# Kernel optimization log

Measured on AMD Instinct MI355X. Metric: run time of the kernel, lower is better.

The kernel has to match this reference:

```python
import jax, jax.numpy as jnp
import numpy as np

B, N, K, F = 1, 50000, 16, 128
EPS = 1e-5

def _bn(h, gamma, beta):
    # BatchNorm1d in training mode: per-feature-channel stats over (batch, nodes)
    mean = jnp.mean(h, axis=(0, 1), keepdims=True)
    var = jnp.var(h, axis=(0, 1), keepdims=True)
    return (h - mean) * jax.lax.rsqrt(var + EPS) * gamma + beta

def _rgcn(h, neighbors, W, b):
    # pad one zero node row, gather K neighbors per node, flatten, linear
    h_pad = jnp.pad(h, ((0, 0), (0, 1), (0, 0)))           # [B, N+1, F]
    gathered = h_pad[:, neighbors]                          # [B, N, K, F]
    flat = gathered.reshape(h.shape[0], neighbors.shape[0], -1)  # [B, N, K*F]
    return jnp.einsum('bnk,ok->bno', flat, W) + b

def setup_inputs():
    key = jax.random.key(0)
    ks = jax.random.split(key, 10)
    x = jax.random.normal(ks[0], (B, N, F), jnp.float32)
    graph = jax.random.randint(ks[1], (N, K, 2), 0, N)
    gamma1 = 1.0 + 0.1 * jax.random.normal(ks[2], (F,), jnp.float32)
    beta1 = 0.1 * jax.random.normal(ks[3], (F,), jnp.float32)
    gamma2 = 1.0 + 0.1 * jax.random.normal(ks[4], (F,), jnp.float32)
    beta2 = 0.1 * jax.random.normal(ks[5], (F,), jnp.float32)
    s = 1.0 / np.sqrt(K * F)
    W1 = jax.random.uniform(ks[6], (F, K * F), jnp.float32, -s, s)
    b1 = jax.random.uniform(ks[7], (F,), jnp.float32, -s, s)
    W2 = jax.random.uniform(ks[8], (F, K * F), jnp.float32, -s, s)
    b2 = jax.random.uniform(ks[9], (F,), jnp.float32, -s, s)
    return {"x": x, "graph": graph, "gamma1": gamma1, "beta1": beta1,
            "W1": W1, "b1": b1, "gamma2": gamma2, "beta2": beta2,
            "W2": W2, "b2": b2}

def reference(x, graph, gamma1, beta1, W1, b1, gamma2, beta2, W2, b2):
    neighbors = graph[..., 1]                               # [N, K]
    out = jax.nn.gelu(_bn(x, gamma1, beta1), approximate=False)
    out = _rgcn(out, neighbors, W1, b1)                     # [B, N, F]
    out = jax.nn.gelu(_bn(out, gamma2, beta2), approximate=False)
    out = _rgcn(out, neighbors, W2, b2)                     # [B, N, F]
    return out + x
```

## Files before the change

kernel.cpp:

```cpp
#include <hip/hip_runtime.h>


#define NN  50000
#define NB  500
#define NPB 100

typedef __bf16 v8bf __attribute__((ext_vector_type(8)));
typedef unsigned short u8s __attribute__((ext_vector_type(8)));
typedef float  v4f  __attribute__((ext_vector_type(4)));
typedef float  vf2  __attribute__((ext_vector_type(2)));

__device__ __forceinline__ unsigned short f2bf(float f) {
  unsigned int u = __builtin_bit_cast(unsigned int, f);
  u += 0x7FFFu + ((u >> 16) & 1u);
  return (unsigned short)(u >> 16);
}
__device__ __forceinline__ float bf2f(unsigned short s) {
  unsigned int u = ((unsigned int)s) << 16;
  return __builtin_bit_cast(float, u);
}
__device__ __forceinline__ float gelu_f(float y) {
  return 0.5f * y * (1.0f + erff(y * 0.70710678118654752f));
}

__device__ __forceinline__ v8bf fp8x8_to_bf16x8(unsigned int lo, unsigned int hi) {
  vf2 f0 = __builtin_amdgcn_cvt_pk_f32_fp8((int)lo, false);
  vf2 f1 = __builtin_amdgcn_cvt_pk_f32_fp8((int)lo, true);
  vf2 f2 = __builtin_amdgcn_cvt_pk_f32_fp8((int)hi, false);
  vf2 f3 = __builtin_amdgcn_cvt_pk_f32_fp8((int)hi, true);
  unsigned int d0, d1, d2, d3;
  asm("v_cvt_pk_bf16_f32 %0, %1, %2" : "=v"(d0) : "v"(f0.x), "v"(f0.y));
  asm("v_cvt_pk_bf16_f32 %0, %1, %2" : "=v"(d1) : "v"(f1.x), "v"(f1.y));
  asm("v_cvt_pk_bf16_f32 %0, %1, %2" : "=v"(d2) : "v"(f2.x), "v"(f2.y));
  asm("v_cvt_pk_bf16_f32 %0, %1, %2" : "=v"(d3) : "v"(f3.x), "v"(f3.y));
  uint4 u = make_uint4(d0, d1, d2, d3);
  return __builtin_bit_cast(v8bf, u);
}

__global__ void wconv_kernel(const float* __restrict__ W1, const float* __restrict__ W2,
                             unsigned short* __restrict__ Wt1, unsigned short* __restrict__ Wt2) {
  int t = blockIdx.x * 256 + threadIdx.x;
  const bool is2 = (t >= 32768);
  const float* W = is2 ? W2 : W1;
  unsigned short* Wt = is2 ? Wt2 : Wt1;
  int r = t & 32767;
  int frag = r >> 6, lane = r & 63;
  int k4 = frag >> 3, c = frag & 7;
  int o  = c * 16 + (lane & 15);
  int lq = lane >> 4;
  int kd;
  if (!is2) {
    kd = k4 * 32 + lq * 8;
  } else {
    int s_ = k4 >> 2, w_ = k4 & 3;
    kd = s_ * 128 + (w_ >> 1) * 64 + lq * 16 + (w_ & 1) * 8;
  }
  const float* src = W + o * 2048 + kd;
  unsigned short* dst = Wt + r * 8;
#pragma unroll
  for (int j = 0; j < 8; ++j) dst[j] = f2bf(src[j]);
}

__global__ void bn_stats_kernel(const float* __restrict__ x, float* __restrict__ part) {
  float s0=0,s1=0,s2=0,s3=0,q0=0,q1=0,q2=0,q3=0;
  for (int cb = blockIdx.x; cb < (NN*128/1024); cb += 256) {
    float4 v = reinterpret_cast<const float4*>(x)[cb * 256 + threadIdx.x];
    s0+=v.x; q0+=v.x*v.x; s1+=v.y; q1+=v.y*v.y;
    s2+=v.z; q2+=v.z*v.z; s3+=v.w; q3+=v.w*v.w;
  }
  __shared__ float ls[1024], lsq[1024];
  int fb = (threadIdx.x & 31) * 4;
  int sl = threadIdx.x >> 5;
  ls[sl*128+fb]   = s0; ls[sl*128+fb+1]  = s1; ls[sl*128+fb+2]  = s2; ls[sl*128+fb+3]  = s3;
  lsq[sl*128+fb]  = q0; lsq[sl*128+fb+1] = q1; lsq[sl*128+fb+2] = q2; lsq[sl*128+fb+3] = q3;
  __syncthreads();
  if (threadIdx.x < 128) {
    float S=0,Q=0;
#pragma unroll
    for (int s2i=0; s2i<8; ++s2i){ S += ls[s2i*128+threadIdx.x]; Q += lsq[s2i*128+threadIdx.x]; }
    part[blockIdx.x*256 + threadIdx.x]       = S;
    part[blockIdx.x*256 + 128 + threadIdx.x] = Q;
  }
}

__global__ __launch_bounds__(1024) void bn_reduce_kernel(
    const float* __restrict__ part, int nb,
    const float* __restrict__ gamma, const float* __restrict__ beta,
    float* __restrict__ scsh) {
  int f = threadIdx.x & 127;
  int g = threadIdx.x >> 7;
  float S = 0.f, Q = 0.f;
  for (int b = g; b < nb; b += 8) {
    S += part[b * 256 + f];
    Q += part[b * 256 + 128 + f];
  }
  __shared__ float ls[8][128], lq[8][128];
  ls[g][f] = S; lq[g][f] = Q;
  __syncthreads();
  if (threadIdx.x < 128) {
    float St = 0.f, Qt = 0.f;
#pragma unroll
    for (int i = 0; i < 8; ++i) { St += ls[i][f]; Qt += lq[i][f]; }
    float inv  = 1.0f / (float)NN;
    float mean = St * inv;
    float var  = fmaxf(Qt * inv - mean * mean, 0.0f);
    float sc   = gamma[f] * rsqrtf(var + 1e-5f);
    scsh[f]       = sc;
    scsh[128 + f] = beta[f] - mean * sc;
  }
}

__global__ void apply1_kernel(const float* __restrict__ x, const float* __restrict__ scsh,
                              unsigned short* __restrict__ h1) {
  int stride = gridDim.x * blockDim.x;
  for (int c = blockIdx.x * blockDim.x + threadIdx.x; c < NN*128/4; c += stride) {
    float4 v = reinterpret_cast<const float4*>(x)[c];
    int f = (c * 4) & 127;
    ushort4 o;
    o.x = f2bf(gelu_f(v.x * scsh[f]   + scsh[128+f]));
    o.y = f2bf(gelu_f(v.y * scsh[f+1] + scsh[128+f+1]));
    o.z = f2bf(gelu_f(v.z * scsh[f+2] + scsh[128+f+2]));
    o.w = f2bf(gelu_f(v.w * scsh[f+3] + scsh[128+f+3]));
    reinterpret_cast<ushort4*>(h1)[c] = o;
  }
}

__global__ void apply2_kernel(const unsigned short* __restrict__ t1,
                              const float* __restrict__ scsh,
                              unsigned int* __restrict__ h2) {
  int stride = gridDim.x * blockDim.x;
  for (int c = blockIdx.x * blockDim.x + threadIdx.x; c < NN*128/8; c += stride) {
    u8s v = reinterpret_cast<const u8s*>(t1)[c];
    int f = (c * 8) & 127;
    float r[8];
#pragma unroll
    for (int j = 0; j < 8; ++j)
      r[j] = gelu_f(bf2f((unsigned short)v[j]) * scsh[f + j] + scsh[128 + f + j]);
    int lo = __builtin_amdgcn_cvt_pk_fp8_f32(r[0], r[1], 0,  false);
    lo     = __builtin_amdgcn_cvt_pk_fp8_f32(r[2], r[3], lo, true);
    int hi = __builtin_amdgcn_cvt_pk_fp8_f32(r[4], r[5], 0,  false);
    hi     = __builtin_amdgcn_cvt_pk_fp8_f32(r[6], r[7], hi, true);
    reinterpret_cast<uint2*>(h2)[c] = make_uint2((unsigned)lo, (unsigned)hi);
  }
}

template<int MODE>
__global__ __launch_bounds__(256, 2) void rgcn_kernel(
    const void* __restrict__ hb,
    const unsigned short* __restrict__ Wt,
    const int* __restrict__ graph,
    const float* __restrict__ bias,
    const float* __restrict__ xres,
    float* __restrict__ outf,
    unsigned short* __restrict__ outb,
    float* __restrict__ part)
{
  __shared__ unsigned short bsm[16384];
  __shared__ float lds_s[4][128];
  __shared__ float lds_q[4][128];

  const unsigned short* h16 = (const unsigned short*)hb;
  const unsigned char*  h8  = (const unsigned char*)hb;

  const int tid  = threadIdx.x;
  const int wv   = tid >> 6;
  const int lane = tid & 63;
  const int l15  = lane & 15;
  const int lq   = lane >> 4;
  const int nb0  = blockIdx.x * NPB;

  v4f acc[2][8];
#pragma unroll
  for (int rf = 0; rf < 2; ++rf)
#pragma unroll
    for (int c = 0; c < 8; ++c) acc[rf][c] = (v4f){0.f, 0.f, 0.f, 0.f};

  const int an0 = min(nb0 + wv * 32 + l15,      NN - 1);
  const int an1 = min(nb0 + wv * 32 + 16 + l15, NN - 1);

  int idx0[16], idx1[16];
  {
    const int4* g0 = reinterpret_cast<const int4*>(graph + an0 * 32);
    const int4* g1 = reinterpret_cast<const int4*>(graph + an1 * 32);
#pragma unroll
    for (int j = 0; j < 8; ++j) {
      int4 t0 = g0[j], t1v = g1[j];
      idx0[2*j]   = min(max(t0.y,  0), NN - 1) * 128;
      idx0[2*j+1] = min(max(t0.w,  0), NN - 1) * 128;
      idx1[2*j]   = min(max(t1v.y, 0), NN - 1) * 128;
      idx1[2*j+1] = min(max(t1v.w, 0), NN - 1) * 128;
    }
  }

  v8bf  A0[2][4],  A1[2][4];
  uint4 A0u[2][2], A1u[2][2];

#define LOADA(buf_, s_) {                                                 \
    if constexpr (MODE == 0) {                                            \
      const unsigned short* r0 = h16 + idx0[s_] + lq * 8;                 \
      const unsigned short* r1 = h16 + idx1[s_] + lq * 8;                 \
      _Pragma("unroll")                                                   \
      for (int w4 = 0; w4 < 4; ++w4) {                                    \
        A0[buf_][w4] = *reinterpret_cast<const v8bf*>(r0 + w4 * 32);      \
        A1[buf_][w4] = *reinterpret_cast<const v8bf*>(r1 + w4 * 32);      \
      }                                                                   \
    } else {                                                              \
      const unsigned char* r0 = h8 + idx0[s_] + lq * 16;                  \
      const unsigned char* r1 = h8 + idx1[s_] + lq * 16;                  \
      A0u[buf_][0] = *reinterpret_cast<const uint4*>(r0);                 \
      A0u[buf_][1] = *reinterpret_cast<const uint4*>(r0 + 64);            \
      A1u[buf_][0] = *reinterpret_cast<const uint4*>(r1);                 \
      A1u[buf_][1] = *reinterpret_cast<const uint4*>(r1 + 64);            \
    }                                                                     \
  }

#define STAGE(s_) {                                                           \
    const unsigned short* gsrc = Wt + (s_) * 16384 + wv * 4096 + lane * 8;    \
    unsigned short* ldst = &bsm[wv * 4096];                                   \
    _Pragma("unroll")                                                         \
    for (int i = 0; i < 8; ++i) {                                             \
      __builtin_amdgcn_global_load_lds(                                       \
        (const __attribute__((address_space(1))) void*)(gsrc + i * 512),      \
        (__attribute__((address_space(3))) void*)(ldst + i * 512),            \
        16, 0, 0);                                                            \
    }                                                                         \
  }

#define SLOT(s_) {                                                            \
    if ((s_) < 15) LOADA(((s_) + 1) & 1, ((s_) + 1) & 15)                     \
    __builtin_amdgcn_sched_barrier(0);                                        \
    __builtin_amdgcn_s_setprio(1);                                            \
    {                                                                         \
      const int cur_ = (s_) & 1;                                              \
      _Pragma("unroll")                                                       \
      for (int w4 = 0; w4 < 4; ++w4) {                                        \
        v8bf a0v, a1v;                                                        \
        if constexpr (MODE == 0) {                                            \
          a0v = A0[cur_][w4];                                                 \
          a1v = A1[cur_][w4];                                                 \
        } else {                                                              \
          uint4 u0 = A0u[cur_][w4 >> 1];                                      \
          uint4 u1 = A1u[cur_][w4 >> 1];                                      \
          if ((w4 & 1) == 0) {                                                \
            a0v = fp8x8_to_bf16x8(u0.x, u0.y);                                \
            a1v = fp8x8_to_bf16x8(u1.x, u1.y);                                \
          } else {                                                            \
            a0v = fp8x8_to_bf16x8(u0.z, u0.w);                                \
            a1v = fp8x8_to_bf16x8(u1.z, u1.w);                                \
          }                                                                   \
        }                                                                     \
        _Pragma("unroll")                                                     \
        for (int c = 0; c < 8; ++c) {                                         \
          v8bf b = *reinterpret_cast<const v8bf*>(                            \
              &bsm[(w4 * 8 + c) * 512 + lane * 8]);                           \
          acc[0][c] = __builtin_amdgcn_mfma_f32_16x16x32_bf16(                \
                        a0v, b, acc[0][c], 0, 0, 0);                          \
          acc[1][c] = __builtin_amdgcn_mfma_f32_16x16x32_bf16(                \
                        a1v, b, acc[1][c], 0, 0, 0);                          \
        }                                                                     \
      }                                                                       \
    }                                                                         \
    __builtin_amdgcn_s_setprio(0);                                            \
    __builtin_amdgcn_sched_barrier(0);                                        \
    __builtin_amdgcn_s_barrier();             \
    __builtin_amdgcn_sched_barrier(0);                                        \
    if ((s_) < 15) STAGE(((s_) + 1) & 15)                                     \
    __syncthreads();                      \
  }

  STAGE(0)
  LOADA(0, 0)
  __syncthreads();

  SLOT(0)  SLOT(1)  SLOT(2)  SLOT(3)
  SLOT(4)  SLOT(5)  SLOT(6)  SLOT(7)
  SLOT(8)  SLOT(9)  SLOT(10) SLOT(11)
  SLOT(12) SLOT(13) SLOT(14) SLOT(15)
#undef SLOT
#undef LOADA
#undef STAGE

  if constexpr (MODE == 0) {
#pragma unroll
    for (int c = 0; c < 8; ++c) {
      float s = 0.f, q = 0.f;
#pragma unroll
      for (int rf = 0; rf < 2; ++rf) {
#pragma unroll
        for (int j = 0; j < 4; ++j) {
          int lrow = wv * 32 + rf * 16 + lq * 4 + j;
          float v  = acc[rf][c][j];
          if (lrow < NPB) { s += v; q += v * v; }
          bsm[lrow * 128 + c * 16 + l15] = f2bf(v);
        }
      }
      s += __shfl_xor(s, 16, 64); s += __shfl_xor(s, 32, 64);
      q += __shfl_xor(q, 16, 64); q += __shfl_xor(q, 32, 64);
      if (lq == 0) { lds_s[wv][c * 16 + l15] = s; lds_q[wv][c * 16 + l15] = q; }
    }
    __syncthreads();
    unsigned short* t1b = outb + nb0 * 128;
#pragma unroll
    for (int i = 0; i < 7; ++i) {
      int off = i * 2048 + tid * 8;
      if (off < NPB * 128) {
        *reinterpret_cast<u8s*>(t1b + off) =
            *reinterpret_cast<const u8s*>(&bsm[off]);
      }
    }
    if (tid < 128) {
      float S = lds_s[0][tid] + lds_s[1][tid] + lds_s[2][tid] + lds_s[3][tid];
      float Q = lds_q[0][tid] + lds_q[1][tid] + lds_q[2][tid] + lds_q[3][tid];
      part[blockIdx.x * 256 + tid]       = S;
      part[blockIdx.x * 256 + 128 + tid] = Q;
    }
  } else {
#pragma unroll
    for (int c = 0; c < 8; ++c) {
      float bv = bias[c * 16 + l15];
#pragma unroll
      for (int rf = 0; rf < 2; ++rf) {
#pragma unroll
        for (int j = 0; j < 4; ++j) {
          int node = nb0 + wv * 32 + rf * 16 + lq * 4 + j;
          if (node < nb0 + NPB) {
            int idx = node * 128 + c * 16 + l15;
            outf[idx] = acc[rf][c][j] + bv + xres[idx];
          }
        }
      }
    }
  }
}

extern "C" void kernel_launch(void* const* d_in, const int* in_sizes, int n_in,
                              void* d_out, int out_size, void* d_ws, size_t ws_size,
                              hipStream_t stream) {
  const float* x      = (const float*)d_in[0];
  const int*   graph  = (const int*)d_in[1];
  const float* gamma1 = (const float*)d_in[2];
  const float* beta1  = (const float*)d_in[3];
  const float* W1     = (const float*)d_in[4];
  const float* gamma2 = (const float*)d_in[6];
  const float* beta2  = (const float*)d_in[7];
  const float* W2     = (const float*)d_in[8];
  const float* b2     = (const float*)d_in[9];
  float* out = (float*)d_out;

  char* ws = (char*)d_ws;
  unsigned short* h1  = (unsigned short*)(ws);
  unsigned short* t1  = (unsigned short*)(ws + 12800000);
  unsigned short* Wt1 = (unsigned short*)(ws + 25600000);
  unsigned short* Wt2 = (unsigned short*)(ws + 26124288);
  float* p1    = (float*)(ws + 26648576);
  float* p2    = (float*)(ws + 26910720);
  float* scsh1 = (float*)(ws + 27422720);
  float* scsh2 = (float*)(ws + 27423744);

  wconv_kernel<<<256, 256, 0, stream>>>(W1, W2, Wt1, Wt2);
  bn_stats_kernel<<<256, 256, 0, stream>>>(x, p1);
  bn_reduce_kernel<<<1, 1024, 0, stream>>>(p1, 256, gamma1, beta1, scsh1);
  apply1_kernel<<<2048, 256, 0, stream>>>(x, scsh1, h1);
  rgcn_kernel<0><<<NB, 256, 0, stream>>>(h1, Wt1, graph, nullptr, nullptr,
                                         nullptr, t1, p2);
  bn_reduce_kernel<<<1, 1024, 0, stream>>>(p2, NB, gamma2, beta2, scsh2);
  apply2_kernel<<<2048, 256, 0, stream>>>(t1, scsh2, (unsigned int*)h1);
  rgcn_kernel<1><<<NB, 256, 0, stream>>>(h1, Wt2, graph, b2, x,
                                         out, nullptr, nullptr);
}
```

Before: 201.3 us.

## Store first-layer activations in FP8 and process two neighbor slots per pipeline phase

The first GELU output is now stored as FP8 instead of bf16, so both RGCN layers share the FP8 gather path and weight layout. This halves the bytes of the random neighbor gathers in layer one. The main loop now handles two neighbor slots per phase with a doubled LDS weight buffer, which halves the number of barriers and stage steps. The cost is lower precision in the first layer's inputs and 64KB of LDS per block, which may reduce occupancy below the two blocks per CU the launch bounds request.

Measured after the change: 203.6 us. No clear change (+1.2%).

```diff
diff --git a/kernel.cpp b/kernel.cpp
--- a/kernel.cpp
+++ b/kernel.cpp
@@ -48,13 +48,8 @@
   int k4 = frag >> 3, c = frag & 7;
   int o  = c * 16 + (lane & 15);
   int lq = lane >> 4;
-  int kd;
-  if (!is2) {
-    kd = k4 * 32 + lq * 8;
-  } else {
-    int s_ = k4 >> 2, w_ = k4 & 3;
-    kd = s_ * 128 + (w_ >> 1) * 64 + lq * 16 + (w_ & 1) * 8;
-  }
+  int s_ = k4 >> 2, w_ = k4 & 3;
+  int kd = s_ * 128 + (w_ >> 1) * 64 + lq * 16 + (w_ & 1) * 8;
   const float* src = W + o * 2048 + kd;
   unsigned short* dst = Wt + r * 8;
 #pragma unroll
@@ -111,17 +106,21 @@
 }
 
 __global__ void apply1_kernel(const float* __restrict__ x, const float* __restrict__ scsh,
-                              unsigned short* __restrict__ h1) {
+                              unsigned int* __restrict__ h1) {
   int stride = gridDim.x * blockDim.x;
-  for (int c = blockIdx.x * blockDim.x + threadIdx.x; c < NN*128/4; c += stride) {
-    float4 v = reinterpret_cast<const float4*>(x)[c];
-    int f = (c * 4) & 127;
-    ushort4 o;
-    o.x = f2bf(gelu_f(v.x * scsh[f]   + scsh[128+f]));
-    o.y = f2bf(gelu_f(v.y * scsh[f+1] + scsh[128+f+1]));
-    o.z = f2bf(gelu_f(v.z * scsh[f+2] + scsh[128+f+2]));
-    o.w = f2bf(gelu_f(v.w * scsh[f+3] + scsh[128+f+3]));
-    reinterpret_cast<ushort4*>(h1)[c] = o;
+  for (int c = blockIdx.x * blockDim.x + threadIdx.x; c < NN*128/8; c += stride) {
+    float4 v0 = reinterpret_cast<const float4*>(x)[c * 2];
+    float4 v1 = reinterpret_cast<const float4*>(x)[c * 2 + 1];
+    int f = (c * 8) & 127;
+    float r[8] = {v0.x, v0.y, v0.z, v0.w, v1.x, v1.y, v1.z, v1.w};
+#pragma unroll
+    for (int j = 0; j < 8; ++j)
+      r[j] = gelu_f(r[j] * scsh[f + j] + scsh[128 + f + j]);
+    int lo = __builtin_amdgcn_cvt_pk_fp8_f32(r[0], r[1], 0,  false);
+    lo     = __builtin_amdgcn_cvt_pk_fp8_f32(r[2], r[3], lo, true);
+    int hi = __builtin_amdgcn_cvt_pk_fp8_f32(r[4], r[5], 0,  false);
+    hi     = __builtin_amdgcn_cvt_pk_fp8_f32(r[6], r[7], hi, true);
+    reinterpret_cast<uint2*>(h1)[c] = make_uint2((unsigned)lo, (unsigned)hi);
   }
 }
 
@@ -146,7 +145,7 @@
 
 template<int MODE>
 __global__ __launch_bounds__(256, 2) void rgcn_kernel(
-    const void* __restrict__ hb,
+    const unsigned char* __restrict__ h8,
     const unsigned short* __restrict__ Wt,
     const int* __restrict__ graph,
     const float* __restrict__ bias,
@@ -155,12 +154,9 @@
     unsigned short* __restrict__ outb,
     float* __restrict__ part)
 {
-  __shared__ unsigned short bsm[16384];
+  __shared__ unsigned short bsm[32768];
   __shared__ float lds_s[4][128];
   __shared__ float lds_q[4][128];
-
-  const unsigned short* h16 = (const unsigned short*)hb;
-  const unsigned char*  h8  = (const unsigned char*)hb;
 
   const int tid  = threadIdx.x;
   const int wv   = tid >> 6;
@@ -192,33 +188,25 @@
     }
   }
 
-  v8bf  A0[2][4],  A1[2][4];
-  uint4 A0u[2][2], A1u[2][2];
-
-#define LOADA(buf_, s_) {                                                 \
-    if constexpr (MODE == 0) {                                            \
-      const unsigned short* r0 = h16 + idx0[s_] + lq * 8;                 \
-      const unsigned short* r1 = h16 + idx1[s_] + lq * 8;                 \
-      _Pragma("unroll")                                                   \
-      for (int w4 = 0; w4 < 4; ++w4) {                                    \
-        A0[buf_][w4] = *reinterpret_cast<const v8bf*>(r0 + w4 * 32);      \
-        A1[buf_][w4] = *reinterpret_cast<const v8bf*>(r1 + w4 * 32);      \
-      }                                                                   \
-    } else {                                                              \
-      const unsigned char* r0 = h8 + idx0[s_] + lq * 16;                  \
-      const unsigned char* r1 = h8 + idx1[s_] + lq * 16;                  \
-      A0u[buf_][0] = *reinterpret_cast<const uint4*>(r0);                 \
-      A0u[buf_][1] = *reinterpret_cast<const uint4*>(r0 + 64);            \
-      A1u[buf_][0] = *reinterpret_cast<const uint4*>(r1);                 \
-      A1u[buf_][1] = *reinterpret_cast<const uint4*>(r1 + 64);            \
+  uint4 A0u[2][2][2], A1u[2][2][2];
+
+#define LOADA2(buf_, p_) {                                                \
+    _Pragma("unroll")                                                     \
+    for (int sl = 0; sl < 2; ++sl) {                                      \
+      const unsigned char* r0 = h8 + idx0[(p_) * 2 + sl] + lq * 16;       \
+      const unsigned char* r1 = h8 + idx1[(p_) * 2 + sl] + lq * 16;       \
+      A0u[buf_][sl][0] = *reinterpret_cast<const uint4*>(r0);             \
+      A0u[buf_][sl][1] = *reinterpret_cast<const uint4*>(r0 + 64);        \
+      A1u[buf_][sl][0] = *reinterpret_cast<const uint4*>(r1);             \
+      A1u[buf_][sl][1] = *reinterpret_cast<const uint4*>(r1 + 64);        \
     }                                                                     \
   }
 
-#define STAGE(s_) {                                                           \
-    const unsigned short* gsrc = Wt + (s_) * 16384 + wv * 4096 + lane * 8;    \
-    unsigned short* ldst = &bsm[wv * 4096];                                   \
+#define STAGE2(p_) {                                                          \
+    const unsigned short* gsrc = Wt + (p_) * 32768 + wv * 8192 + lane * 8;    \
+    unsigned short* ldst = &bsm[wv * 8192];                                   \
     _Pragma("unroll")                                                         \
-    for (int i = 0; i < 8; ++i) {                                             \
+    for (int i = 0; i < 16; ++i) {                                            \
       __builtin_amdgcn_global_load_lds(                                       \
         (const __attribute__((address_space(1))) void*)(gsrc + i * 512),      \
         (__attribute__((address_space(3))) void*)(ldst + i * 512),            \
@@ -226,21 +214,19 @@
     }                                                                         \
   }
 
-#define SLOT(s_) {                                                            \
-    if ((s_) < 15) LOADA(((s_) + 1) & 1, ((s_) + 1) & 15)                     \
+#define PHASE(p_) {                                                           \
+    if ((p_) < 7) LOADA2(((p_) + 1) & 1, ((p_) + 1) & 7)                      \
     __builtin_amdgcn_sched_barrier(0);                                        \
     __builtin_amdgcn_s_setprio(1);                                            \
     {                                                                         \
-      const int cur_ = (s_) & 1;                                              \
+      const int cur_ = (p_) & 1;                                              \
       _Pragma("unroll")                                                       \
-      for (int w4 = 0; w4 < 4; ++w4) {                                        \
-        v8bf a0v, a1v;                                                        \
-        if constexpr (MODE == 0) {                                            \
-          a0v = A0[cur_][w4];                                                 \
-          a1v = A1[cur_][w4];                                                 \
-        } else {                                                              \
-          uint4 u0 = A0u[cur_][w4 >> 1];                                      \
-          uint4 u1 = A1u[cur_][w4 >> 1];                                      \
+      for (int sl = 0; sl < 2; ++sl) {                                        \
+        _Pragma("unroll")                                                     \
+        for (int w4 = 0; w4 < 4; ++w4) {                                      \
+          uint4 u0 = A0u[cur_][sl][w4 >> 1];                                  \
+          uint4 u1 = A1u[cur_][sl][w4 >> 1];                                  \
+          v8bf a0v, a1v;                                                      \
           if ((w4 & 1) == 0) {                                                \
             a0v = fp8x8_to_bf16x8(u0.x, u0.y);                                \
             a1v = fp8x8_to_bf16x8(u1.x, u1.y);                                \
@@ -248,15 +234,15 @@
             a0v = fp8x8_to_bf16x8(u0.z, u0.w);                                \
             a1v = fp8x8_to_bf16x8(u1.z, u1.w);                                \
           }                                                                   \
-        }                                                                     \
-        _Pragma("unroll")                                                     \
-        for (int c = 0; c < 8; ++c) {                                         \
-          v8bf b = *reinterpret_cast<const v8bf*>(                            \
-              &bsm[(w4 * 8 + c) * 512 + lane * 8]);                           \
-          acc[0][c] = __builtin_amdgcn_mfma_f32_16x16x32_bf16(                \
-                        a0v, b, acc[0][c], 0, 0, 0);                          \
-          acc[1][c] = __builtin_amdgcn_mfma_f32_16x16x32_bf16(                \
-                        a1v, b, acc[1][c], 0, 0, 0);                          \
+          _Pragma("unroll")                                                   \
+          for (int c = 0; c < 8; ++c) {                                       \
+            v8bf b = *reinterpret_cast<const v8bf*>(                          \
+                &bsm[sl * 16384 + (w4 * 8 + c) * 512 + lane * 8]);            \
+            acc[0][c] = __builtin_amdgcn_mfma_f32_16x16x32_bf16(              \
+                          a0v, b, acc[0][c], 0, 0, 0);                        \
+            acc[1][c] = __builtin_amdgcn_mfma_f32_16x16x32_bf16(              \
+                          a1v, b, acc[1][c], 0, 0, 0);                        \
+          }                                                                   \
         }                                                                     \
       }                                                                       \
     }                                                                         \
@@ -264,21 +250,19 @@
     __builtin_amdgcn_sched_barrier(0);                                        \
     __builtin_amdgcn_s_barrier();             \
     __builtin_amdgcn_sched_barrier(0);                                        \
-    if ((s_) < 15) STAGE(((s_) + 1) & 15)                                     \
+    if ((p_) < 7) STAGE2(((p_) + 1) & 7)                                      \
     __syncthreads();                      \
   }
 
-  STAGE(0)
-  LOADA(0, 0)
+  STAGE2(0)
+  LOADA2(0, 0)
   __syncthreads();
 
-  SLOT(0)  SLOT(1)  SLOT(2)  SLOT(3)
-  SLOT(4)  SLOT(5)  SLOT(6)  SLOT(7)
-  SLOT(8)  SLOT(9)  SLOT(10) SLOT(11)
-  SLOT(12) SLOT(13) SLOT(14) SLOT(15)
-#undef SLOT
-#undef LOADA
-#undef STAGE
+  PHASE(0)  PHASE(1)  PHASE(2)  PHASE(3)
+  PHASE(4)  PHASE(5)  PHASE(6)  PHASE(7)
+#undef PHASE
+#undef LOADA2
+#undef STAGE2
 
   if constexpr (MODE == 0) {
 #pragma unroll
@@ -348,7 +332,7 @@
   float* out = (float*)d_out;
 
   char* ws = (char*)d_ws;
-  unsigned short* h1  = (unsigned short*)(ws);
+  unsigned char*  h1  = (unsigned char*)(ws);
   unsigned short* t1  = (unsigned short*)(ws + 12800000);
   unsigned short* Wt1 = (unsigned short*)(ws + 25600000);
   unsigned short* Wt2 = (unsigned short*)(ws + 26124288);
@@ -360,7 +344,7 @@
   wconv_kernel<<<256, 256, 0, stream>>>(W1, W2, Wt1, Wt2);
   bn_stats_kernel<<<256, 256, 0, stream>>>(x, p1);
   bn_reduce_kernel<<<1, 1024, 0, stream>>>(p1, 256, gamma1, beta1, scsh1);
-  apply1_kernel<<<2048, 256, 0, stream>>>(x, scsh1, h1);
+  apply1_kernel<<<2048, 256, 0, stream>>>(x, scsh1, (unsigned int*)h1);
   rgcn_kernel<0><<<NB, 256, 0, stream>>>(h1, Wt1, graph, nullptr, nullptr,
                                          nullptr, t1, p2);
   bn_reduce_kernel<<<1, 1024, 0, stream>>>(p2, NB, gamma2, beta2, scsh2);
```
